# Optimization experiments

Hardware: AMD Instinct MI355X
Metric: run time of the kernel (lower is better)

## Reference

```python
import jax, jax.numpy as jnp
import numpy as np

B, N, M = 4, 1024, 1024
PFD, AD, GFD = 1024, 256, 512
H, DH = 4, 64
NR, CUT = 16, 2.0
SCALE = DH ** -0.5
OFFSETS = jnp.linspace(0.0, CUT, NR)
COEFF = -0.5 / (CUT / (NR - 1)) ** 2


def _ln(x, g, b, eps=1e-5):
    mu = x.mean(-1, keepdims=True)
    var = ((x - mu) ** 2).mean(-1, keepdims=True)
    return (x - mu) / jnp.sqrt(var + eps) * g + b


def _kabsch(src, tgt, w):
    # weighted Kabsch: rotation/translation aligning src -> tgt
    w = w / (w.sum(-1, keepdims=True) + 1e-8)  # (B,N)
    cs = jnp.einsum('bn,bnc->bc', w, src)
    ct = jnp.einsum('bn,bnc->bc', w, tgt)
    sc = src - cs[:, None]
    tc = tgt - ct[:, None]
    Hm = jnp.einsum('bn,bnc,bnd->bcd', w, sc, tc)  # (B,3,3)
    U, _, Vt = jnp.linalg.svd(Hm)
    V = jnp.swapaxes(Vt, -1, -2)
    d = jnp.linalg.det(V @ jnp.swapaxes(U, -1, -2))
    D = jnp.stack([jnp.ones_like(d), jnp.ones_like(d), d], -1)  # (B,3)
    R = jnp.einsum('bij,bj,bkj->bik', V, D, U)
    t = ct - jnp.einsum('bij,bj->bi', R, cs)
    return R, t


def setup_inputs():
    key = jax.random.key(0)
    it = iter(jax.random.split(key, 48))
    nrm = lambda s, sc=1.0: jax.random.normal(next(it), s, jnp.float32) * sc
    return {
        'src_point_feats': nrm((B, N, PFD)),
        'tgt_point_feats': nrm((B, M, PFD)),
        'src_points': nrm((B, N, 3)),
        'tgt_points': nrm((B, M, 3)),
        'tgt_global': nrm((B, GFD)),
        'sfp_w': nrm((PFD, AD), 0.02), 'sfp_b': jnp.zeros((AD,)), 'sfp_g': jnp.ones((AD,)), 'sfp_bb': jnp.zeros((AD,)),
        'tfp_w': nrm((PFD, AD), 0.02), 'tfp_b': jnp.zeros((AD,)), 'tfp_g': jnp.ones((AD,)), 'tfp_bb': jnp.zeros((AD,)),
        'rbf_w': nrm((NR, H), 0.1),
        'qw': nrm((AD, AD), 0.02), 'qb': jnp.zeros((AD,)),
        'kw': nrm((AD, AD), 0.02), 'kb': jnp.zeros((AD,)),
        'vw': nrm((AD, AD), 0.02), 'vb': jnp.zeros((AD,)),
        'ow': nrm((AD, AD), 0.02), 'ob': jnp.zeros((AD,)),
        'n1_g': jnp.ones((AD,)), 'n1_b': jnp.zeros((AD,)),
        'f1_w': nrm((AD, 4 * AD), 0.02), 'f1_b': jnp.zeros((4 * AD,)),
        'f2_w': nrm((4 * AD, AD), 0.02), 'f2_b': jnp.zeros((AD,)),
        'n2_g': jnp.ones((AD,)), 'n2_b': jnp.zeros((AD,)),
        'scp_w': nrm((AD, AD), 0.02), 'scp_b': jnp.zeros((AD,)),
        'tcp_w': nrm((AD, AD), 0.02), 'tcp_b': jnp.zeros((AD,)),
        'temperature': jnp.array(0.05, jnp.float32),
        'gp_w': nrm((AD, GFD), 0.02), 'gp_b': jnp.zeros((GFD,)), 'gp_g': jnp.ones((GFD,)), 'gp_bb': jnp.zeros((GFD,)),
    }


def reference(src_point_feats, tgt_point_feats, src_points, tgt_points, tgt_global,
              sfp_w, sfp_b, sfp_g, sfp_bb, tfp_w, tfp_b, tfp_g, tfp_bb, rbf_w,
              qw, qb, kw, kb, vw, vb, ow, ob, n1_g, n1_b,
              f1_w, f1_b, f2_w, f2_b, n2_g, n2_b,
              scp_w, scp_b, tcp_w, tcp_b, temperature,
              gp_w, gp_b, gp_g, gp_bb):
    # feature projections
    src_proj = jax.nn.relu(_ln(src_point_feats @ sfp_w + sfp_b, sfp_g, sfp_bb))  # (B,N,AD)
    tgt_proj = jax.nn.relu(_ln(tgt_point_feats @ tfp_w + tfp_b, tfp_g, tfp_bb))  # (B,M,AD)
    # inter-cloud geometric bias: cdist -> gaussian RBF -> per-head linear (dist no-grad)
    d2 = ((src_points ** 2).sum(-1)[:, :, None] + (tgt_points ** 2).sum(-1)[:, None, :]
          - 2.0 * jnp.einsum('bnc,bmc->bnm', src_points, tgt_points))
    dist = jnp.sqrt(jnp.clip(d2, 0.0))  # (B,N,M)
    rbf = jnp.exp(COEFF * (dist[..., None] - OFFSETS) ** 2)  # (B,N,M,NR)
    rbf = jax.lax.stop_gradient(rbf)
    bias = jnp.einsum('bnmr,rh->bhnm', rbf, rbf_w)
    # cross attention with geo bias (pre-LN on both streams, shared LN params)
    xq = _ln(src_proj, n1_g, n1_b)
    xc = _ln(tgt_proj, n1_g, n1_b)
    q = (xq @ qw + qb).reshape(B, N, H, DH)
    k = (xc @ kw + kb).reshape(B, M, H, DH)
    v = (xc @ vw + vb).reshape(B, M, H, DH)
    logits = jnp.einsum('bnhd,bmhd->bhnm', q, k) * SCALE + bias
    p = jax.nn.softmax(logits, axis=-1)
    attn_out = jnp.einsum('bhnm,bmhd->bnhd', p, v).reshape(B, N, AD) @ ow + ob
    x = src_proj + attn_out
    # FFN block (exact GELU as in torch)
    h = _ln(x, n2_g, n2_b)
    x = x + (jax.nn.gelu(h @ f1_w + f1_b, approximate=False) @ f2_w + f2_b)
    # soft correspondences + 3-step log-domain Sinkhorn
    src_corr = x @ scp_w + scp_b
    tgt_corr = tgt_proj @ tcp_w + tcp_b
    tau = jnp.clip(temperature, 0.01, 1.0)
    logS = jnp.einsum('bnd,bmd->bnm', src_corr, tgt_corr) / tau
    for _ in range(3):
        logS = logS - jax.nn.logsumexp(logS, axis=-1, keepdims=True)
        logS = logS - jax.nn.logsumexp(logS, axis=-2, keepdims=True)
    S = jnp.exp(logS)
    tgt_corr_points = jnp.einsum('bnm,bmc->bnc', S, tgt_points)
    confidence = S.max(-1)
    R_res, t_res = _kabsch(src_points, tgt_corr_points, confidence)
    src_global_new = jax.nn.relu(_ln(x.max(1) @ gp_w + gp_b, gp_g, gp_bb))
    combined = jnp.concatenate([src_global_new, tgt_global], axis=-1)
    return R_res, t_res, combined, confidence, S
```

## Files before the change

### kernel.cpp

```cpp
#include <hip/hip_runtime.h>
#include <hip/hip_bf16.h>
#include <math.h>

constexpr int Bn  = 4;
constexpr int Nn  = 1024;
constexpr int Mmm = 1024;
constexpr int PFDc = 1024;
constexpr int ADc  = 256;
constexpr int GFDc = 512;
constexpr int Hc   = 4;
constexpr int NRc  = 16;
constexpr int NSPLIT = 32;
constexpr float COEFFc = -28.125f;
constexpr float SCALEc = 0.125f;
constexpr float STEPc  = 2.0f / 15.0f;

__device__ __forceinline__ float addf(float a, float b) { return a + b; }
__device__ __forceinline__ double addd(double a, double b) { return a + b; }

#define BLK_REDUCE_F(OP, VAR, RES) \
  red[tid] = (VAR); __syncthreads(); \
  for (int st_ = 128; st_ > 0; st_ >>= 1) { if (tid < st_) red[tid] = OP(red[tid], red[tid + st_]); __syncthreads(); } \
  (RES) = red[0]; __syncthreads();

// ... 54 lines not shown
      float v = acc[i][j] + bias[c];
      if (addsrc) v += addsrc[(size_t)r * Cc + c];
      if (act == 1) v = 0.5f * v * (1.f + erff(v * 0.70710678118654752f));
      C[(size_t)r * Cc + c] = v;
    }
  }
}

__global__ __launch_bounds__(256) void gemm256_k(
    const float* __restrict__ A, const float* __restrict__ W, const float* __restrict__ bias,
    const float* __restrict__ addsrc, float* __restrict__ C,
    int R, int K, int Cc, int act)
{
  __shared__ __align__(16) float As[2][16][68];
  __shared__ __align__(16) float Ws[2][16][68];
  const int tid = threadIdx.x;
  const int tx = tid & 15, ty = tid >> 4;
  const int r0 = blockIdx.y * 64, c0 = blockIdx.x * 64;
  float acc[4][4] = {};
  float ra[4], rb[4];

  #pragma unroll
  for (int j = 0; j < 4; ++j) {
    int e = tid + j * 256;
    ra[j] = A[(size_t)(r0 + (e >> 4)) * K + (e & 15)];
    rb[j] = W[(size_t)(e >> 6) * Cc + c0 + (e & 63)];
  }
  #pragma unroll
  for (int j = 0; j < 4; ++j) {
    int e = tid + j * 256;
    As[0][e & 15][e >> 4] = ra[j];
    Ws[0][e >> 6][e & 63] = rb[j];
  }
  __syncthreads();

  const int nstep = K >> 4;
  for (int s = 0; s < nstep; ++s) {
    const int cur = s & 1;
    if (s + 1 < nstep) {
      const int k0 = (s + 1) << 4;
      #pragma unroll
      for (int j = 0; j < 4; ++j) {
        int e = tid + j * 256;
        ra[j] = A[(size_t)(r0 + (e >> 4)) * K + k0 + (e & 15)];
        rb[j] = W[(size_t)(k0 + (e >> 6)) * Cc + c0 + (e & 63)];
      }
    }
    #pragma unroll
    for (int kk = 0; kk < 16; ++kk) {
      float4 av = *(const float4*)&As[cur][kk][ty * 4];
      float4 wv = *(const float4*)&Ws[cur][kk][tx * 4];
      float a[4] = {av.x, av.y, av.z, av.w};
      float w[4] = {wv.x, wv.y, wv.z, wv.w};
      #pragma unroll
      for (int i = 0; i < 4; ++i)
        #pragma unroll
        for (int j = 0; j < 4; ++j)
          acc[i][j] = fmaf(a[i], w[j], acc[i][j]);
    }
    if (s + 1 < nstep) {
      #pragma unroll
      for (int j = 0; j < 4; ++j) {
        int e = tid + j * 256;
        As[cur ^ 1][e & 15][e >> 4] = ra[j];
        Ws[cur ^ 1][e >> 6][e & 63] = rb[j];
      }
    }
    __syncthreads();
  }
  #pragma unroll
  for (int i = 0; i < 4; ++i) {
    int r = r0 + ty * 4 + i;
    #pragma unroll
    for (int j = 0; j < 4; ++j) {
      int c = c0 + tx * 4 + j;
      float v = acc[i][j] + bias[c];
      if (addsrc) v += addsrc[(size_t)r * Cc + c];
      if (act == 1) v = 0.5f * v * (1.f + erff(v * 0.70710678118654752f));
      C[(size_t)r * Cc + c] = v;
    }
  }
}

__global__ __launch_bounds__(256) void gemm128_k(
    const float* __restrict__ A, const float* __restrict__ W, const float* __restrict__ bias,
    const float* __restrict__ addsrc, float* __restrict__ C,
    int R, int K, int Cc, int act)
{
  __shared__ __align__(16) float As[2][8][132];
  __shared__ __align__(16) float Ws[2][8][132];
  const int tid = threadIdx.x;
  const int tx = tid & 15, ty = tid >> 4;
  const int r0 = blockIdx.y * 128, c0 = blockIdx.x * 128;
  float acc[8][8] = {};
  float ra[4], rb[4];

  #pragma unroll
  for (int j = 0; j < 4; ++j) {
    int e = tid + j * 256;
    ra[j] = A[(size_t)(r0 + (e >> 3)) * K + (e & 7)];
    rb[j] = W[(size_t)(e >> 7) * Cc + c0 + (e & 127)];
  }
  #pragma unroll
  for (int j = 0; j < 4; ++j) {
    int e = tid + j * 256;
    As[0][e & 7][e >> 3] = ra[j];
    Ws[0][e >> 7][e & 127] = rb[j];
  }
  __syncthreads();

  const int nstep = K >> 3;
  for (int s = 0; s < nstep; ++s) {
    const int cur = s & 1;
    if (s + 1 < nstep) {
      const int k0 = (s + 1) << 3;
      #pragma unroll
      for (int j = 0; j < 4; ++j) {
        int e = tid + j * 256;
        ra[j] = A[(size_t)(r0 + (e >> 3)) * K + k0 + (e & 7)];
        rb[j] = W[(size_t)(k0 + (e >> 7)) * Cc + c0 + (e & 127)];
      }
    }
    #pragma unroll
    for (int kk = 0; kk < 8; ++kk) {
      float a[8], w[8];
      *(float4*)&a[0] = *(const float4*)&As[cur][kk][ty * 8];
      *(float4*)&a[4] = *(const float4*)&As[cur][kk][ty * 8 + 4];
      *(float4*)&w[0] = *(const float4*)&Ws[cur][kk][tx * 8];
      *(float4*)&w[4] = *(const float4*)&Ws[cur][kk][tx * 8 + 4];
      #pragma unroll
      for (int i = 0; i < 8; ++i)
        #pragma unroll
        for (int j = 0; j < 8; ++j)
          acc[i][j] = fmaf(a[i], w[j], acc[i][j]);
    }
    if (s + 1 < nstep) {
      #pragma unroll
      for (int j = 0; j < 4; ++j) {
        int e = tid + j * 256;
        As[cur ^ 1][e & 7][e >> 3] = ra[j];
        Ws[cur ^ 1][e >> 7][e & 127] = rb[j];
      }
    }
    __syncthreads();
  }
  #pragma unroll
  for (int i = 0; i < 8; ++i) {
    int r = r0 + ty * 8 + i;
    #pragma unroll
    for (int j = 0; j < 8; ++j) {
      int c = c0 + tx * 8 + j;
      float v = acc[i][j] + bias[c];
      if (addsrc) v += addsrc[(size_t)r * Cc + c];
      if (act == 1) v = 0.5f * v * (1.f + erff(v * 0.70710678118654752f));
      C[(size_t)r * Cc + c] = v;
    }
  }
}

__global__ __launch_bounds__(256) void gemm_nt128_k(
    const float* __restrict__ A, const float* __restrict__ Bm, float* __restrict__ C,
    const float* __restrict__ temp)
{
  const int K = ADc;
  __shared__ __align__(16) float As[2][8][132];
  __shared__ __align__(16) float Bs[2][8][132];
  const int tid = threadIdx.x;
  const int tx = tid & 15, ty = tid >> 4;
  const int b = blockIdx.z;
  const int r0 = blockIdx.y * 128, c0 = blockIdx.x * 128;
  const float* Ab = A + (size_t)b * Nn * K;
  const float* Bb = Bm + (size_t)b * Mmm * K;
  float* Cb = C + (size_t)b * Nn * Mmm;
  float tau = fminf(fmaxf(temp[0], 0.01f), 1.0f);
  float inv_tau = 1.f / tau;
  float acc[8][8] = {};
  float ra[4], rb[4];

  #pragma unroll
  for (int j = 0; j < 4; ++j) {
    int e = tid + j * 256;
    ra[j] = Ab[(size_t)(r0 + (e >> 3)) * K + (e & 7)];
    rb[j] = Bb[(size_t)(c0 + (e >> 3)) * K + (e & 7)];
  }
  #pragma unroll
  for (int j = 0; j < 4; ++j) {
    int e = tid + j * 256;
    As[0][e & 7][e >> 3] = ra[j];
    Bs[0][e & 7][e >> 3] = rb[j];
  }
  __syncthreads();

  const int nstep = K >> 3;
  for (int s = 0; s < nstep; ++s) {
    const int cur = s & 1;
    if (s + 1 < nstep) {
      const int k0 = (s + 1) << 3;
      #pragma unroll
      for (int j = 0; j < 4; ++j) {
        int e = tid + j * 256;
        ra[j] = Ab[(size_t)(r0 + (e >> 3)) * K + k0 + (e & 7)];
        rb[j] = Bb[(size_t)(c0 + (e >> 3)) * K + k0 + (e & 7)];
      }
    }
    #pragma unroll
    for (int kk = 0; kk < 8; ++kk) {
      float a[8], w[8];
      *(float4*)&a[0] = *(const float4*)&As[cur][kk][ty * 8];
      *(float4*)&a[4] = *(const float4*)&As[cur][kk][ty * 8 + 4];
      *(float4*)&w[0] = *(const float4*)&Bs[cur][kk][tx * 8];
      *(float4*)&w[4] = *(const float4*)&Bs[cur][kk][tx * 8 + 4];
      #pragma unroll
      for (int i = 0; i < 8; ++i)
        #pragma unroll
        for (int j = 0; j < 8; ++j)
          acc[i][j] = fmaf(a[i], w[j], acc[i][j]);
    }
    if (s + 1 < nstep) {
      #pragma unroll
      for (int j = 0; j < 4; ++j) {
        int e = tid + j * 256;
        As[cur ^ 1][e & 7][e >> 3] = ra[j];
        Bs[cur ^ 1][e & 7][e >> 3] = rb[j];
      }
    }
    __syncthreads();
  }
  #pragma unroll
  for (int i = 0; i < 8; ++i) {
    int r = r0 + ty * 8 + i;
    #pragma unroll
    for (int j = 0; j < 8; ++j) {
      int c = c0 + tx * 8 + j;
      Cb[(size_t)r * Mmm + c] = acc[i][j] * inv_tau;
    }
  }
}

__global__ __launch_bounds__(256) void ln_k(
    const float* __restrict__ in, const float* __restrict__ g, const float* __restrict__ bb,
    float* __restrict__ out, int Cc, int relu)
{
  const int tid = threadIdx.x;
  const int row = blockIdx.x;
  const float* x = in + (size_t)row * Cc;
  float* o = out + (size_t)row * Cc;
  __shared__ float red[256];
  float s = 0.f;
  for (int j = tid; j < Cc; j += 256) s += x[j];
  float tot; BLK_REDUCE_F(addf, s, tot);
  float mu = tot / Cc;
  float s2 = 0.f;
  for (int j = tid; j < Cc; j += 256) { float d = x[j] - mu; s2 += d * d; }
  float tot2; BLK_REDUCE_F(addf, s2, tot2);
  float inv = 1.f / sqrtf(tot2 / Cc + 1e-5f);
  for (int j = tid; j < Cc; j += 256) {
    float v = (x[j] - mu) * inv * g[j] + bb[j];
    if (relu) v = fmaxf(v, 0.f);
    o[j] = v;
  }
}

__global__ __launch_bounds__(256) void ln2_k(
    const float* __restrict__ in, const float* __restrict__ g, const float* __restrict__ bb,
    float* __restrict__ out, int relu)
{
  const int row = blockIdx.x;
  const int tid = threadIdx.x;
  float x = in[(size_t)row * 256 + tid];
  float s = x, s2 = x * x;
  #pragma unroll
  for (int off = 32; off > 0; off >>= 1) {
    s  += __shfl_xor(s, off, 64);
    s2 += __shfl_xor(s2, off, 64);
  }
  __shared__ float as_[4], as2_[4];
  const int wv = tid >> 6, ln = tid & 63;
  if (ln == 0) { as_[wv] = s; as2_[wv] = s2; }
  __syncthreads();
  s  = as_[0] + as_[1] + as_[2] + as_[3];
  s2 = as2_[0] + as2_[1] + as2_[2] + as2_[3];
  float mu = s * (1.f / 256.f);
  float var = fmaxf(s2 * (1.f / 256.f) - mu * mu, 0.f);
  float inv = 1.f / sqrtf(var + 1e-5f);
  float v = (x - mu) * inv * g[tid] + bb[tid];
  if (relu) v = fmaxf(v, 0.f);
  out[(size_t)row * 256 + tid] = v;
}

__global__ __launch_bounds__(256) void fattn(
    const float* __restrict__ q, const float* __restrict__ k, const float* __restrict__ v,
    const float* __restrict__ src_pts, const float* __restrict__ tgt_pts,
    const float* __restrict__ rbfw, float* __restrict__ ctx)
{
  const int bh = blockIdx.x;
  const int b = bh >> 2, h = bh & 3;
  const int n0 = blockIdx.y * 32;
  const int tid = threadIdx.x;
  const int tx = tid & 15, ty = tid >> 4;
  const int lane = tid & 63, w = tid >> 6;
  const int mml = lane >> 4;
  const int dd  = lane & 15;

  __shared__ __align__(16) float Qs[64][36];
  __shared__ __align__(16) float Ks[64][68];
  __shared__ __align__(16) float Vs[64][68];
  __shared__ __align__(16) float Ps[32][68];
  __shared__ float spx[32], spy[32], spz[32];
  __shared__ float tpx[64], tpy[64], tpz[64];
  __shared__ float rw[16];

  #pragma unroll
  for (int c = 0; c < 8; ++c) {
    int n = c * 4 + mml;
    int d = w * 16 + dd;
    Qs[d][n] = q[((size_t)b * Nn + n0 + n) * ADc + h * 64 + d];
  }
  if (tid < 32) {
    spx[tid] = src_pts[((size_t)b * Nn + n0 + tid) * 3 + 0];
    spy[tid] = src_pts[((size_t)b * Nn + n0 + tid) * 3 + 1];
    spz[tid] = src_pts[((size_t)b * Nn + n0 + tid) * 3 + 2];
  }
  if (tid < 16) rw[tid] = rbfw[tid * Hc + h];

  float O[2][4] = {};
  float mrun[2] = {-1e30f, -1e30f};
  float lrun[2] = {0.f, 0.f};

  for (int t = 0; t < Mmm / 64; ++t) {
    const int m0 = t * 64;
    __syncthreads();
    #pragma unroll
    for (int c = 0; c < 16; ++c) {
      int mm = c * 4 + mml;
      int d = w * 16 + dd;
      Ks[d][mm] = k[((size_t)b * Mmm + m0 + mm) * ADc + h * 64 + d];
    }
    #pragma unroll
    for (int c = 0; c < 16; ++c) {
      int mm = c * 4 + w;
      Vs[mm][lane] = v[((size_t)b * Mmm + m0 + mm) * ADc + h * 64 + lane];
    }
    if (tid < 64) {
      tpx[tid] = tgt_pts[((size_t)b * Mmm + m0 + tid) * 3 + 0];
      tpy[tid] = tgt_pts[((size_t)b * Mmm + m0 + tid) * 3 + 1];
      tpz[tid] = tgt_pts[((size_t)b * Mmm + m0 + tid) * 3 + 2];
    }
    __syncthreads();

    float S[2][4] = {};
    #pragma unroll
    for (int d = 0; d < 64; ++d) {
      float2 qv = *(const float2*)&Qs[d][ty * 2];
      float4 kv = *(const float4*)&Ks[d][tx * 4];
      float kw[4] = {kv.x, kv.y, kv.z, kv.w};
      #pragma unroll
      for (int j = 0; j < 4; ++j) {
        S[0][j] = fmaf(qv.x, kw[j], S[0][j]);
        S[1][j] = fmaf(qv.y, kw[j], S[1][j]);
      }
    }

    #pragma unroll
    for (int i = 0; i < 2; ++i) {
      int n = ty * 2 + i;
      float s0 = spx[n], s1 = spy[n], s2 = spz[n];
      float sq = s0 * s0 + s1 * s1 + s2 * s2;
      float rmx = -1e30f;
      #pragma unroll
      for (int j = 0; j < 4; ++j) {
        int mj = tx * 4 + j;
        float t0 = tpx[mj], t1 = tpy[mj], t2 = tpz[mj];
        float d2 = sq + t0 * t0 + t1 * t1 + t2 * t2 - 2.f * (s0 * t0 + s1 * t1 + s2 * t2);
        float dist = sqrtf(fmaxf(d2, 0.f));
        float bias = 0.f;
        float dq = dist;
        #pragma unroll
        for (int r = 0; r < NRc; ++r) {
          bias = fmaf(__expf(COEFFc * dq * dq), rw[r], bias);
          dq -= STEPc;
        }
        float lv = S[i][j] * SCALEc + bias;
        S[i][j] = lv;
        rmx = fmaxf(rmx, lv);
      }
      #pragma unroll
      for (int off = 1; off < 16; off <<= 1)
        rmx = fmaxf(rmx, __shfl_xor(rmx, off, 64));
      float mn = fmaxf(mrun[i], rmx);
      float alpha = __expf(mrun[i] - mn);
      mrun[i] = mn;
      float p0 = __expf(S[i][0] - mn);
      float p1 = __expf(S[i][1] - mn);
      float p2 = __expf(S[i][2] - mn);
      float p3 = __expf(S[i][3] - mn);
      *(float4*)&Ps[n][tx * 4] = make_float4(p0, p1, p2, p3);
      float rs = p0 + p1 + p2 + p3;
      #pragma unroll
      for (int off = 1; off < 16; off <<= 1)
        rs += __shfl_xor(rs, off, 64);
      lrun[i] = lrun[i] * alpha + rs;
      O[i][0] *= alpha; O[i][1] *= alpha; O[i][2] *= alpha; O[i][3] *= alpha;
    }

    #pragma unroll
    for (int m = 0; m < 64; ++m) {
      float4 vv = *(const float4*)&Vs[m][tx * 4];
      float vw[4] = {vv.x, vv.y, vv.z, vv.w};
      float p0 = Ps[ty * 2][m];
      float p1 = Ps[ty * 2 + 1][m];
      #pragma unroll
      for (int j = 0; j < 4; ++j) {
        O[0][j] = fmaf(p0, vw[j], O[0][j]);
        O[1][j] = fmaf(p1, vw[j], O[1][j]);
      }
    }
  }

  #pragma unroll
  for (int i = 0; i < 2; ++i) {
    int n = n0 + ty * 2 + i;
    float invl = 1.f / lrun[i];
    size_t base = ((size_t)b * Nn + n) * ADc + h * 64 + tx * 4;
    ctx[base + 0] = O[i][0] * invl;
    ctx[base + 1] = O[i][1] * invl;
    ctx[base + 2] = O[i][2] * invl;
    ctx[base + 3] = O[i][3] * invl;
  }
}

__global__ __launch_bounds__(256) void row_lse2_k(float* __restrict__ logS, const float* __restrict__ colLse)
{
  const int tid = threadIdx.x;
  const int bn = blockIdx.x;
  const int b = bn >> 10;
  float* row = logS + (size_t)bn * Mmm;
  float4 v4 = *(float4*)&row[tid * 4];
  if (colLse) {
    const float4 c4 = *(const float4*)&colLse[(size_t)b * Mmm + tid * 4];
    v4.x -= c4.x; v4.y -= c4.y; v4.z -= c4.z; v4.w -= c4.w;
  }
  float mx = fmaxf(fmaxf(v4.x, v4.y), fmaxf(v4.z, v4.w));
  float sm = __expf(v4.x - mx) + __expf(v4.y - mx) + __expf(v4.z - mx) + __expf(v4.w - mx);
  #pragma unroll
  for (int off = 32; off > 0; off >>= 1) {
    float mo = __shfl_xor(mx, off, 64);
    float so = __shfl_xor(sm, off, 64);
    float mn = fmaxf(mx, mo);
    sm = sm * __expf(mx - mn) + so * __expf(mo - mn);
    mx = mn;
  }
  __shared__ float wm[4], wsum[4];
  const int wv = tid >> 6, ln = tid & 63;
  if (ln == 0) { wm[wv] = mx; wsum[wv] = sm; }
  __syncthreads();
  float m0 = fmaxf(fmaxf(wm[0], wm[1]), fmaxf(wm[2], wm[3]));
  float stot = wsum[0] * __expf(wm[0] - m0) + wsum[1] * __expf(wm[1] - m0)
             + wsum[2] * __expf(wm[2] - m0) + wsum[3] * __expf(wm[3] - m0);
  float lse = m0 + __logf(stot);
  v4.x -= lse; v4.y -= lse; v4.z -= lse; v4.w -= lse;
  *(float4*)&row[tid * 4] = v4;
}

__global__ __launch_bounds__(256) void col_part_k(
    const float* __restrict__ logS, float* __restrict__ pmax, float* __restrict__ psum)
{
  const int b = blockIdx.z, sp = blockIdx.y;
  const int m = blockIdx.x * 256 + threadIdx.x;
  const int RPS = Nn / NSPLIT;
  const float* base = logS + ((size_t)b * Nn + sp * RPS) * Mmm + m;
  float mx = -1e30f, sm = 0.f;
  for (int i = 0; i < RPS; ++i) {
    float v = base[(size_t)i * Mmm];
    if (v > mx) { sm = sm * __expf(mx - v) + 1.f; mx = v; }
    else sm += __expf(v - mx);
  }
  size_t o = ((size_t)b * NSPLIT + sp) * Mmm + m;
  pmax[o] = mx; psum[o] = sm;
}

__global__ __launch_bounds__(256) void col_comb_k(
    const float* __restrict__ pmax, const float* __restrict__ psum, float* __restrict__ colLse)
{
  const int b = blockIdx.y;
  const int m = blockIdx.x * 256 + threadIdx.x;
  float mx = -1e30f;
  for (int s = 0; s < NSPLIT; ++s) mx = fmaxf(mx, pmax[((size_t)b * NSPLIT + s) * Mmm + m]);
  float sm = 0.f;
  for (int s = 0; s < NSPLIT; ++s) {
    size_t o = ((size_t)b * NSPLIT + s) * Mmm + m;
    sm += psum[o] * __expf(pmax[o] - mx);
  }
  colLse[(size_t)b * Mmm + m] = mx + __logf(sm);
}

__global__ __launch_bounds__(256) void finalize_k(
    const float* __restrict__ logS, const float* __restrict__ colLse,
// ... 208 lines not shown
  const int b = blockIdx.x, ch = blockIdx.y;
  const int d = threadIdx.x;
  float mx = -1e30f;
  const int n0 = ch * 64;
  for (int n = n0; n < n0 + 64; ++n)
    mx = fmaxf(mx, x[((size_t)b * Nn + n) * ADc + d]);
  part[((size_t)b * 16 + ch) * ADc + d] = mx;
}

__global__ __launch_bounds__(256) void xmax_comb_k(const float* __restrict__ part, float* __restrict__ xmax)
{
  const int b = blockIdx.x, d = threadIdx.x;
  float mx = -1e30f;
  for (int c = 0; c < 16; ++c) mx = fmaxf(mx, part[((size_t)b * 16 + c) * ADc + d]);
  xmax[(size_t)b * ADc + d] = mx;
}

__global__ __launch_bounds__(256) void combined_k(
    const float* __restrict__ gl, const float* __restrict__ tgt_global, float* __restrict__ outC)
{
  int i = blockIdx.x * 256 + threadIdx.x;
  int b = i >> 10, j = i & 1023;
  float v = (j < GFDc) ? gl[(size_t)b * GFDc + j] : tgt_global[(size_t)b * GFDc + (j - GFDc)];
  outC[i] = v;
}

extern "C" void kernel_launch(void* const* d_in, const int* in_sizes, int n_in,
                              void* d_out, int out_size, void* d_ws, size_t ws_size,
                              hipStream_t stream) {
  (void)in_sizes; (void)n_in; (void)out_size; (void)ws_size;
  const float* src_feats = (const float*)d_in[0];
  const float* tgt_feats = (const float*)d_in[1];
  const float* src_pts   = (const float*)d_in[2];
  const float* tgt_pts   = (const float*)d_in[3];
  const float* tgt_glob  = (const float*)d_in[4];
  const float* sfp_w = (const float*)d_in[5];  const float* sfp_b = (const float*)d_in[6];
  const float* sfp_g = (const float*)d_in[7];  const float* sfp_bb = (const float*)d_in[8];
  const float* tfp_w = (const float*)d_in[9];  const float* tfp_b = (const float*)d_in[10];
  const float* tfp_g = (const float*)d_in[11]; const float* tfp_bb = (const float*)d_in[12];
  const float* rbf_w = (const float*)d_in[13];
  const float* qw = (const float*)d_in[14]; const float* qb = (const float*)d_in[15];
  const float* kw = (const float*)d_in[16]; const float* kb = (const float*)d_in[17];
  const float* vw = (const float*)d_in[18]; const float* vb = (const float*)d_in[19];
  const float* ow = (const float*)d_in[20]; const float* ob = (const float*)d_in[21];
  const float* n1_g = (const float*)d_in[22]; const float* n1_b = (const float*)d_in[23];
  const float* f1_w = (const float*)d_in[24]; const float* f1_b = (const float*)d_in[25];
  const float* f2_w = (const float*)d_in[26]; const float* f2_b = (const float*)d_in[27];
  const float* n2_g = (const float*)d_in[28]; const float* n2_b = (const float*)d_in[29];
  const float* scp_w = (const float*)d_in[30]; const float* scp_b = (const float*)d_in[31];
  const float* tcp_w = (const float*)d_in[32]; const float* tcp_b = (const float*)d_in[33];
  const float* temp  = (const float*)d_in[34];
  const float* gp_w = (const float*)d_in[35]; const float* gp_b = (const float*)d_in[36];
  const float* gp_g = (const float*)d_in[37]; const float* gp_bb = (const float*)d_in[38];

  float* out = (float*)d_out;
  float* outR    = out;
  float* outT    = out + 36;
  float* outC    = out + 48;
  float* outConf = out + 48 + 4096;
  float* outS    = out + 48 + 4096 + 4096;

  float* ws = (float*)d_ws;
  const size_t M1 = 1048576;
  float* A_   = ws + 0 * M1;
  float* B_   = ws + 1 * M1;
  float* C_   = ws + 2 * M1;
  float* D_   = ws + 3 * M1;
  float* E_   = ws + 4 * M1;
  float* F_   = ws + 5 * M1;
  float* G_   = ws + 6 * M1;
  float* logS = ws + 0 * M1;
  float* hid  = ws + 1 * M1;
  float* tail = ws + 7 * M1;
  float* colLse = tail;
  float* pmax   = colLse + 4096;
  float* psum   = pmax + 131072;
  float* conf   = psum + 131072;
  float* tcp    = conf + 4096;
  float* xmax   = tcp + 12288;
  float* glraw  = xmax + 1024;
  float* gl     = glraw + 2048;
  double* kab   = (double*)(gl + 2048);
  float* xpart  = (float*)(kab + 64);

  const int BN = Bn * Nn;

  gemm256_k<<<dim3(ADc / 64, BN / 64), 256, 0, stream>>>(src_feats, sfp_w, sfp_b, nullptr, A_, BN, PFDc, ADc, 0);
  ln2_k<<<BN, 256, 0, stream>>>(A_, sfp_g, sfp_bb, G_, 1);
  gemm256_k<<<dim3(ADc / 64, BN / 64), 256, 0, stream>>>(tgt_feats, tfp_w, tfp_b, nullptr, A_, BN, PFDc, ADc, 0);
  ln2_k<<<BN, 256, 0, stream>>>(A_, tfp_g, tfp_bb, F_, 1);

  ln2_k<<<BN, 256, 0, stream>>>(G_, n1_g, n1_b, A_, 0);
  gemm256_k<<<dim3(ADc / 64, BN / 64), 256, 0, stream>>>(A_, qw, qb, nullptr, C_, BN, ADc, ADc, 0);
  ln2_k<<<BN, 256, 0, stream>>>(F_, n1_g, n1_b, B_, 0);
  gemm256_k<<<dim3(ADc / 64, BN / 64), 256, 0, stream>>>(B_, kw, kb, nullptr, E_, BN, ADc, ADc, 0);
  gemm256_k<<<dim3(ADc / 64, BN / 64), 256, 0, stream>>>(B_, vw, vb, nullptr, D_, BN, ADc, ADc, 0);

  fattn<<<dim3(Bn * Hc, Nn / 32), 256, 0, stream>>>(C_, E_, D_, src_pts, tgt_pts, rbf_w, B_);
  gemm256_k<<<dim3(ADc / 64, BN / 64), 256, 0, stream>>>(B_, ow, ob, G_, G_, BN, ADc, ADc, 0);

  ln2_k<<<BN, 256, 0, stream>>>(G_, n2_g, n2_b, A_, 0);
  gemm128_k<<<dim3(1024 / 128, BN / 128), 256, 0, stream>>>(A_, f1_w, f1_b, nullptr, hid, BN, ADc, 1024, 1);
  gemm256_k<<<dim3(ADc / 64, BN / 64), 256, 0, stream>>>(hid, f2_w, f2_b, G_, G_, BN, 1024, ADc, 0);

  gemm256_k<<<dim3(ADc / 64, BN / 64), 256, 0, stream>>>(G_, scp_w, scp_b, nullptr, E_, BN, ADc, ADc, 0);

  xmax_part_k<<<dim3(Bn, 16), 256, 0, stream>>>(G_, xpart);
  xmax_comb_k<<<Bn, 256, 0, stream>>>(xpart, xmax);
  gemm_k<<<dim3(GFDc / 64, 1), 256, 0, stream>>>(xmax, gp_w, gp_b, nullptr, glraw, Bn, ADc, GFDc, 0);
  ln_k<<<Bn, 256, 0, stream>>>(glraw, gp_g, gp_bb, gl, GFDc, 1);
  combined_k<<<(Bn * 2 * GFDc) / 256, 256, 0, stream>>>(gl, tgt_glob, outC);

  gemm256_k<<<dim3(ADc / 64, BN / 64), 256, 0, stream>>>(F_, tcp_w, tcp_b, nullptr, G_, BN, ADc, ADc, 0);
  gemm_nt128_k<<<dim3(Mmm / 128, Nn / 128, Bn), 256, 0, stream>>>(E_, G_, logS, temp);

  for (int it = 0; it < 3; ++it) {
    row_lse2_k<<<BN, 256, 0, stream>>>(logS, it == 0 ? nullptr : colLse);
    col_part_k<<<dim3(Mmm / 256, NSPLIT, Bn), 256, 0, stream>>>(logS, pmax, psum);
    col_comb_k<<<dim3(Mmm / 256, Bn), 256, 0, stream>>>(pmax, psum, colLse);
  }
  finalize_k<<<BN, 256, 0, stream>>>(logS, colLse, tgt_pts, outS, outConf, conf, tcp);

  kabsch_red_k<<<Bn, 256, 0, stream>>>(conf, src_pts, tcp, kab);
  kabsch_svd_k<<<1, 64, 0, stream>>>(kab, outR, outT);
}
```

Before: 828.8 us.

## Split-K projection GEMMs, fuse K/V GEMM, tabulate RBF bias, prefetch attention tiles

The K=1024 GEMMs (input projections and FFN down-projection) become split-K into four partial buffers, which a fused reduce+bias+LayerNorm or reduce+residual kernel then combines. This raises block count for the narrow 256-column outputs. K and V weights are packed once so one GEMM produces both, and the FFN up-projection and Sinkhorn logits GEMM move to 64x64 tiles. The attention kernel replaces the 16-term RBF exp sum with a per-block lookup table and linear interpolation, and register-prefetches the next K/V tile. The cost is extra partial-buffer traffic and a small approximation error in the RBF bias.

```diff
diff --git a/kernel.cpp b/kernel.cpp
--- a/kernel.cpp
+++ b/kernel.cpp
@@ -160,156 +160,198 @@
   }
 }
 
-__global__ __launch_bounds__(256) void gemm128_k(
-    const float* __restrict__ A, const float* __restrict__ W, const float* __restrict__ bias,
-    const float* __restrict__ addsrc, float* __restrict__ C,
-    int R, int K, int Cc, int act)
-{
-  __shared__ __align__(16) float As[2][8][132];
-  __shared__ __align__(16) float Ws[2][8][132];
+__global__ __launch_bounds__(256) void gemm_sk_k(
+    const float* __restrict__ A, const float* __restrict__ W, float* __restrict__ P)
+{
+  __shared__ __align__(16) float As[2][16][68];
+  __shared__ __align__(16) float Ws[2][16][68];
   const int tid = threadIdx.x;
   const int tx = tid & 15, ty = tid >> 4;
-  const int r0 = blockIdx.y * 128, c0 = blockIdx.x * 128;
-  float acc[8][8] = {};
+  const int r0 = blockIdx.y * 64, c0 = blockIdx.x * 64;
+  const int koff = blockIdx.z * 256;
+  float acc[4][4] = {};
   float ra[4], rb[4];
 
   #pragma unroll
   for (int j = 0; j < 4; ++j) {
     int e = tid + j * 256;
-    ra[j] = A[(size_t)(r0 + (e >> 3)) * K + (e & 7)];
-    rb[j] = W[(size_t)(e >> 7) * Cc + c0 + (e & 127)];
+    ra[j] = A[(size_t)(r0 + (e >> 4)) * 1024 + koff + (e & 15)];
+    rb[j] = W[(size_t)(koff + (e >> 6)) * 256 + c0 + (e & 63)];
   }
   #pragma unroll
   for (int j = 0; j < 4; ++j) {
     int e = tid + j * 256;
-    As[0][e & 7][e >> 3] = ra[j];
-    Ws[0][e >> 7][e & 127] = rb[j];
+    As[0][e & 15][e >> 4] = ra[j];
+    Ws[0][e >> 6][e & 63] = rb[j];
   }
   __syncthreads();
 
-  const int nstep = K >> 3;
-  for (int s = 0; s < nstep; ++s) {
+  for (int s = 0; s < 16; ++s) {
     const int cur = s & 1;
-    if (s + 1 < nstep) {
-      const int k0 = (s + 1) << 3;
+    if (s + 1 < 16) {
+      const int k0 = koff + ((s + 1) << 4);
       #pragma unroll
       for (int j = 0; j < 4; ++j) {
         int e = tid + j * 256;
-        ra[j] = A[(size_t)(r0 + (e >> 3)) * K + k0 + (e & 7)];
-        rb[j] = W[(size_t)(k0 + (e >> 7)) * Cc + c0 + (e & 127)];
-      }
-    }
-    #pragma unroll
-    for (int kk = 0; kk < 8; ++kk) {
-      float a[8], w[8];
-      *(float4*)&a[0] = *(const float4*)&As[cur][kk][ty * 8];
-      *(float4*)&a[4] = *(const float4*)&As[cur][kk][ty * 8 + 4];
-      *(float4*)&w[0] = *(const float4*)&Ws[cur][kk][tx * 8];
-      *(float4*)&w[4] = *(const float4*)&Ws[cur][kk][tx * 8 + 4];
-      #pragma unroll
-      for (int i = 0; i < 8; ++i)
+        ra[j] = A[(size_t)(r0 + (e >> 4)) * 1024 + k0 + (e & 15)];
+        rb[j] = W[(size_t)(k0 + (e >> 6)) * 256 + c0 + (e & 63)];
+      }
+    }
+    #pragma unroll
+    for (int kk = 0; kk < 16; ++kk) {
+      float4 av = *(const float4*)&As[cur][kk][ty * 4];
+      float4 wv = *(const float4*)&Ws[cur][kk][tx * 4];
+      float a[4] = {av.x, av.y, av.z, av.w};
+      float w[4] = {wv.x, wv.y, wv.z, wv.w};
+      #pragma unroll
+      for (int i = 0; i < 4; ++i)
         #pragma unroll
-        for (int j = 0; j < 8; ++j)
+        for (int j = 0; j < 4; ++j)
           acc[i][j] = fmaf(a[i], w[j], acc[i][j]);
     }
-    if (s + 1 < nstep) {
+    if (s + 1 < 16) {
       #pragma unroll
       for (int j = 0; j < 4; ++j) {
         int e = tid + j * 256;
-        As[cur ^ 1][e & 7][e >> 3] = ra[j];
-        Ws[cur ^ 1][e >> 7][e & 127] = rb[j];
+        As[cur ^ 1][e & 15][e >> 4] = ra[j];
+        Ws[cur ^ 1][e >> 6][e & 63] = rb[j];
       }
     }
     __syncthreads();
   }
-  #pragma unroll
-  for (int i = 0; i < 8; ++i) {
-    int r = r0 + ty * 8 + i;
-    #pragma unroll
-    for (int j = 0; j < 8; ++j) {
-      int c = c0 + tx * 8 + j;
-      float v = acc[i][j] + bias[c];
-      if (addsrc) v += addsrc[(size_t)r * Cc + c];
-      if (act == 1) v = 0.5f * v * (1.f + erff(v * 0.70710678118654752f));
-      C[(size_t)r * Cc + c] = v;
-    }
-  }
-}
-
-__global__ __launch_bounds__(256) void gemm_nt128_k(
+  float* Pz = P + (size_t)blockIdx.z * 1048576;
+  #pragma unroll
+  for (int i = 0; i < 4; ++i) {
+    int r = r0 + ty * 4 + i;
+    #pragma unroll
+    for (int j = 0; j < 4; ++j)
+      Pz[(size_t)r * 256 + c0 + tx * 4 + j] = acc[i][j];
+  }
+}
+
+__global__ __launch_bounds__(256) void ln4_k(
+    const float* __restrict__ p, const float* __restrict__ bias,
+    const float* __restrict__ g, const float* __restrict__ bb,
+    float* __restrict__ out, int relu)
+{
+  const int row = blockIdx.x;
+  const int tid = threadIdx.x;
+  size_t o = (size_t)row * 256 + tid;
+  float x = p[o] + p[o + 1048576] + p[o + 2097152] + p[o + 3145728] + bias[tid];
+  float s = x, s2 = x * x;
+  #pragma unroll
+  for (int off = 32; off > 0; off >>= 1) {
+    s  += __shfl_xor(s, off, 64);
+    s2 += __shfl_xor(s2, off, 64);
+  }
+  __shared__ float as_[4], as2_[4];
+  const int wv = tid >> 6, ln = tid & 63;
+  if (ln == 0) { as_[wv] = s; as2_[wv] = s2; }
+  __syncthreads();
+  s  = as_[0] + as_[1] + as_[2] + as_[3];
+  s2 = as2_[0] + as2_[1] + as2_[2] + as2_[3];
+  float mu = s * (1.f / 256.f);
+  float var = fmaxf(s2 * (1.f / 256.f) - mu * mu, 0.f);
+  float inv = 1.f / sqrtf(var + 1e-5f);
+  float v = (x - mu) * inv * g[tid] + bb[tid];
+  if (relu) v = fmaxf(v, 0.f);
+  out[o] = v;
+}
+
+__global__ __launch_bounds__(256) void red4_k(
+    const float* __restrict__ p, const float* __restrict__ bias, float* __restrict__ out)
+{
+  size_t i = (size_t)blockIdx.x * 256 + threadIdx.x;
+  out[i] += p[i] + p[i + 1048576] + p[i + 2097152] + p[i + 3145728] + bias[threadIdx.x];
+}
+
+__global__ __launch_bounds__(256) void pack_kv_k(
+    const float* __restrict__ kw, const float* __restrict__ kb,
+    const float* __restrict__ vw, const float* __restrict__ vb,
+    float* __restrict__ kvw, float* __restrict__ kvb)
+{
+  int i = blockIdx.x * 256 + threadIdx.x;
+  if (i < 256 * 512) {
+    int r = i >> 9, c = i & 511;
+    kvw[i] = (c < 256) ? kw[r * 256 + c] : vw[r * 256 + (c - 256)];
+  } else if (i < 256 * 512 + 512) {
+    int c = i - 256 * 512;
+    kvb[c] = (c < 256) ? kb[c] : vb[c - 256];
+  }
+}
+
+__global__ __launch_bounds__(256) void gemm_nt256_k(
     const float* __restrict__ A, const float* __restrict__ Bm, float* __restrict__ C,
     const float* __restrict__ temp)
 {
   const int K = ADc;
-  __shared__ __align__(16) float As[2][8][132];
-  __shared__ __align__(16) float Bs[2][8][132];
+  __shared__ __align__(16) float As[2][16][68];
+  __shared__ __align__(16) float Bs[2][16][68];
   const int tid = threadIdx.x;
   const int tx = tid & 15, ty = tid >> 4;
   const int b = blockIdx.z;
-  const int r0 = blockIdx.y * 128, c0 = blockIdx.x * 128;
+  const int r0 = blockIdx.y * 64, c0 = blockIdx.x * 64;
   const float* Ab = A + (size_t)b * Nn * K;
   const float* Bb = Bm + (size_t)b * Mmm * K;
   float* Cb = C + (size_t)b * Nn * Mmm;
   float tau = fminf(fmaxf(temp[0], 0.01f), 1.0f);
   float inv_tau = 1.f / tau;
-  float acc[8][8] = {};
+  float acc[4][4] = {};
   float ra[4], rb[4];
 
   #pragma unroll
   for (int j = 0; j < 4; ++j) {
     int e = tid + j * 256;
-    ra[j] = Ab[(size_t)(r0 + (e >> 3)) * K + (e & 7)];
-    rb[j] = Bb[(size_t)(c0 + (e >> 3)) * K + (e & 7)];
+    ra[j] = Ab[(size_t)(r0 + (e >> 4)) * K + (e & 15)];
+    rb[j] = Bb[(size_t)(c0 + (e >> 4)) * K + (e & 15)];
   }
   #pragma unroll
   for (int j = 0; j < 4; ++j) {
     int e = tid + j * 256;
-    As[0][e & 7][e >> 3] = ra[j];
-    Bs[0][e & 7][e >> 3] = rb[j];
+    As[0][e & 15][e >> 4] = ra[j];
+    Bs[0][e & 15][e >> 4] = rb[j];
   }
   __syncthreads();
 
-  const int nstep = K >> 3;
-  for (int s = 0; s < nstep; ++s) {
+  for (int s = 0; s < 16; ++s) {
     const int cur = s & 1;
-    if (s + 1 < nstep) {
-      const int k0 = (s + 1) << 3;
+    if (s + 1 < 16) {
+      const int k0 = (s + 1) << 4;
       #pragma unroll
       for (int j = 0; j < 4; ++j) {
         int e = tid + j * 256;
-        ra[j] = Ab[(size_t)(r0 + (e >> 3)) * K + k0 + (e & 7)];
-        rb[j] = Bb[(size_t)(c0 + (e >> 3)) * K + k0 + (e & 7)];
-      }
-    }
-    #pragma unroll
-    for (int kk = 0; kk < 8; ++kk) {
-      float a[8], w[8];
-      *(float4*)&a[0] = *(const float4*)&As[cur][kk][ty * 8];
-      *(float4*)&a[4] = *(const float4*)&As[cur][kk][ty * 8 + 4];
-      *(float4*)&w[0] = *(const float4*)&Bs[cur][kk][tx * 8];
-      *(float4*)&w[4] = *(const float4*)&Bs[cur][kk][tx * 8 + 4];
-      #pragma unroll
-      for (int i = 0; i < 8; ++i)
+        ra[j] = Ab[(size_t)(r0 + (e >> 4)) * K + k0 + (e & 15)];
+        rb[j] = Bb[(size_t)(c0 + (e >> 4)) * K + k0 + (e & 15)];
+      }
+    }
+    #pragma unroll
+    for (int kk = 0; kk < 16; ++kk) {
+      float4 av = *(const float4*)&As[cur][kk][ty * 4];
+      float4 wv = *(const float4*)&Bs[cur][kk][tx * 4];
+      float a[4] = {av.x, av.y, av.z, av.w};
+      float w[4] = {wv.x, wv.y, wv.z, wv.w};
+      #pragma unroll
+      for (int i = 0; i < 4; ++i)
         #pragma unroll
-        for (int j = 0; j < 8; ++j)
+        for (int j = 0; j < 4; ++j)
           acc[i][j] = fmaf(a[i], w[j], acc[i][j]);
     }
-    if (s + 1 < nstep) {
+    if (s + 1 < 16) {
       #pragma unroll
       for (int j = 0; j < 4; ++j) {
         int e = tid + j * 256;
-        As[cur ^ 1][e & 7][e >> 3] = ra[j];
-        Bs[cur ^ 1][e & 7][e >> 3] = rb[j];
+        As[cur ^ 1][e & 15][e >> 4] = ra[j];
+        Bs[cur ^ 1][e & 15][e >> 4] = rb[j];
       }
     }
     __syncthreads();
   }
   #pragma unroll
-  for (int i = 0; i < 8; ++i) {
-    int r = r0 + ty * 8 + i;
-    #pragma unroll
-    for (int j = 0; j < 8; ++j) {
-      int c = c0 + tx * 8 + j;
+  for (int i = 0; i < 4; ++i) {
+    int r = r0 + ty * 4 + i;
+    #pragma unroll
+    for (int j = 0; j < 4; ++j) {
+      int c = c0 + tx * 4 + j;
       Cb[(size_t)r * Mmm + c] = acc[i][j] * inv_tau;
     }
   }
@@ -367,7 +409,7 @@
 }
 
 __global__ __launch_bounds__(256) void fattn(
-    const float* __restrict__ q, const float* __restrict__ k, const float* __restrict__ v,
+    const float* __restrict__ q, const float* __restrict__ kv,
     const float* __restrict__ src_pts, const float* __restrict__ tgt_pts,
     const float* __restrict__ rbfw, float* __restrict__ ctx)
 {
@@ -387,7 +429,9 @@
   __shared__ float spx[32], spy[32], spz[32];
   __shared__ float tpx[64], tpy[64], tpz[64];
   __shared__ float rw[16];
-
+  __shared__ float Tb[2048];
+
+  if (tid < 16) rw[tid] = rbfw[tid * Hc + h];
   #pragma unroll
   for (int c = 0; c < 8; ++c) {
     int n = c * 4 + mml;
@@ -399,30 +443,59 @@
     spy[tid] = src_pts[((size_t)b * Nn + n0 + tid) * 3 + 1];
     spz[tid] = src_pts[((size_t)b * Nn + n0 + tid) * 3 + 2];
   }
-  if (tid < 16) rw[tid] = rbfw[tid * Hc + h];
+  __syncthreads();
+
+  for (int i = tid; i < 2048; i += 256) {
+    float di = (float)i * (1.0f / 512.0f);
+    float s = 0.f;
+    #pragma unroll
+    for (int r = 0; r < NRc; ++r) {
+      float dq = di - STEPc * r;
+      s = fmaf(__expf(COEFFc * dq * dq), rw[r], s);
+    }
+    Tb[i] = s;
+  }
+
+  float kreg[16], vreg[16];
+  float tp0 = 0.f, tp1 = 0.f, tp2 = 0.f;
+  {
+    const size_t kb_ = ((size_t)b * Mmm) * 512 + h * 64;
+    #pragma unroll
+    for (int c = 0; c < 16; ++c) {
+      kreg[c] = kv[kb_ + (size_t)(c * 4 + mml) * 512 + w * 16 + dd];
+      vreg[c] = kv[kb_ + (size_t)(c * 4 + w) * 512 + 256 + lane];
+    }
+    if (tid < 64) {
+      tp0 = tgt_pts[((size_t)b * Mmm + tid) * 3 + 0];
+      tp1 = tgt_pts[((size_t)b * Mmm + tid) * 3 + 1];
+      tp2 = tgt_pts[((size_t)b * Mmm + tid) * 3 + 2];
+    }
+  }
 
   float O[2][4] = {};
   float mrun[2] = {-1e30f, -1e30f};
   float lrun[2] = {0.f, 0.f};
 
   for (int t = 0; t < Mmm / 64; ++t) {
-    const int m0 = t * 64;
     __syncthreads();
     #pragma unroll
-    for (int c = 0; c < 16; ++c) {
-      int mm = c * 4 + mml;
-      int d = w * 16 + dd;
-      Ks[d][mm] = k[((size_t)b * Mmm + m0 + mm) * ADc + h * 64 + d];
-    }
-    #pragma unroll
-    for (int c = 0; c < 16; ++c) {
-      int mm = c * 4 + w;
-      Vs[mm][lane] = v[((size_t)b * Mmm + m0 + mm) * ADc + h * 64 + lane];
-    }
-    if (tid < 64) {
-      tpx[tid] = tgt_pts[((size_t)b * Mmm + m0 + tid) * 3 + 0];
-      tpy[tid] = tgt_pts[((size_t)b * Mmm + m0 + tid) * 3 + 1];
-      tpz[tid] = tgt_pts[((size_t)b * Mmm + m0 + tid) * 3 + 2];
+    for (int c = 0; c < 16; ++c) Ks[w * 16 + dd][c * 4 + mml] = kreg[c];
+    #pragma unroll
+    for (int c = 0; c < 16; ++c) Vs[c * 4 + w][lane] = vreg[c];
+    if (tid < 64) { tpx[tid] = tp0; tpy[tid] = tp1; tpz[tid] = tp2; }
+    if (t + 1 < Mmm / 64) {
+      const size_t kb_ = ((size_t)b * Mmm + (t + 1) * 64) * 512 + h * 64;
+      #pragma unroll
+      for (int c = 0; c < 16; ++c) {
+        kreg[c] = kv[kb_ + (size_t)(c * 4 + mml) * 512 + w * 16 + dd];
+        vreg[c] = kv[kb_ + (size_t)(c * 4 + w) * 512 + 256 + lane];
+      }
+      if (tid < 64) {
+        size_t tb_ = ((size_t)b * Mmm + (t + 1) * 64 + tid) * 3;
+        tp0 = tgt_pts[tb_ + 0];
+        tp1 = tgt_pts[tb_ + 1];
+        tp2 = tgt_pts[tb_ + 2];
+      }
     }
     __syncthreads();
 
@@ -430,12 +503,12 @@
     #pragma unroll
     for (int d = 0; d < 64; ++d) {
       float2 qv = *(const float2*)&Qs[d][ty * 2];
-      float4 kv = *(const float4*)&Ks[d][tx * 4];
-      float kw[4] = {kv.x, kv.y, kv.z, kv.w};
+      float4 kv4 = *(const float4*)&Ks[d][tx * 4];
+      float kwv[4] = {kv4.x, kv4.y, kv4.z, kv4.w};
       #pragma unroll
       for (int j = 0; j < 4; ++j) {
-        S[0][j] = fmaf(qv.x, kw[j], S[0][j]);
-        S[1][j] = fmaf(qv.y, kw[j], S[1][j]);
+        S[0][j] = fmaf(qv.x, kwv[j], S[0][j]);
+        S[1][j] = fmaf(qv.y, kwv[j], S[1][j]);
       }
     }
 
@@ -451,13 +524,12 @@
         float t0 = tpx[mj], t1 = tpy[mj], t2 = tpz[mj];
         float d2 = sq + t0 * t0 + t1 * t1 + t2 * t2 - 2.f * (s0 * t0 + s1 * t1 + s2 * t2);
         float dist = sqrtf(fmaxf(d2, 0.f));
-        float bias = 0.f;
-        float dq = dist;
-        #pragma unroll
-        for (int r = 0; r < NRc; ++r) {
-          bias = fmaf(__expf(COEFFc * dq * dq), rw[r], bias);
-          dq -= STEPc;
-        }
+        float fidx = fminf(dist * 512.0f, 2047.0f);
+        int i0 = (int)fidx;
+        i0 = (i0 > 2046) ? 2046 : i0;
+        float frac = fidx - (float)i0;
+        float b0 = Tb[i0];
+        float bias = fmaf(Tb[i0 + 1] - b0, frac, b0);
         float lv = S[i][j] * SCALEc + bias;
         S[i][j] = lv;
         rmx = fmaxf(rmx, lv);
@@ -484,13 +556,13 @@
     #pragma unroll
     for (int m = 0; m < 64; ++m) {
       float4 vv = *(const float4*)&Vs[m][tx * 4];
-      float vw[4] = {vv.x, vv.y, vv.z, vv.w};
+      float vwv[4] = {vv.x, vv.y, vv.z, vv.w};
       float p0 = Ps[ty * 2][m];
       float p1 = Ps[ty * 2 + 1][m];
       #pragma unroll
       for (int j = 0; j < 4; ++j) {
-        O[0][j] = fmaf(p0, vw[j], O[0][j]);
-        O[1][j] = fmaf(p1, vw[j], O[1][j]);
+        O[0][j] = fmaf(p0, vwv[j], O[0][j]);
+        O[1][j] = fmaf(p1, vwv[j], O[1][j]);
       }
     }
   }
@@ -865,28 +937,32 @@
   float* gl     = glraw + 2048;
   double* kab   = (double*)(gl + 2048);
   float* xpart  = (float*)(kab + 64);
+  float* kvw    = pmax;
+  float* kvb    = psum;
 
   const int BN = Bn * Nn;
 
-  gemm256_k<<<dim3(ADc / 64, BN / 64), 256, 0, stream>>>(src_feats, sfp_w, sfp_b, nullptr, A_, BN, PFDc, ADc, 0);
-  ln2_k<<<BN, 256, 0, stream>>>(A_, sfp_g, sfp_bb, G_, 1);
-  gemm256_k<<<dim3(ADc / 64, BN / 64), 256, 0, stream>>>(tgt_feats, tfp_w, tfp_b, nullptr, A_, BN, PFDc, ADc, 0);
-  ln2_k<<<BN, 256, 0, stream>>>(A_, tfp_g, tfp_bb, F_, 1);
+  pack_kv_k<<<514, 256, 0, stream>>>(kw, kb, vw, vb, kvw, kvb);
+
+  gemm_sk_k<<<dim3(4, 64, 4), 256, 0, stream>>>(src_feats, sfp_w, outS);
+  ln4_k<<<BN, 256, 0, stream>>>(outS, sfp_b, sfp_g, sfp_bb, G_, 1);
+  gemm_sk_k<<<dim3(4, 64, 4), 256, 0, stream>>>(tgt_feats, tfp_w, outS);
+  ln4_k<<<BN, 256, 0, stream>>>(outS, tfp_b, tfp_g, tfp_bb, F_, 1);
 
   ln2_k<<<BN, 256, 0, stream>>>(G_, n1_g, n1_b, A_, 0);
-  gemm256_k<<<dim3(ADc / 64, BN / 64), 256, 0, stream>>>(A_, qw, qb, nullptr, C_, BN, ADc, ADc, 0);
+  gemm256_k<<<dim3(4, 64), 256, 0, stream>>>(A_, qw, qb, nullptr, C_, BN, ADc, ADc, 0);
   ln2_k<<<BN, 256, 0, stream>>>(F_, n1_g, n1_b, B_, 0);
-  gemm256_k<<<dim3(ADc / 64, BN / 64), 256, 0, stream>>>(B_, kw, kb, nullptr, E_, BN, ADc, ADc, 0);
-  gemm256_k<<<dim3(ADc / 64, BN / 64), 256, 0, stream>>>(B_, vw, vb, nullptr, D_, BN, ADc, ADc, 0);
-
-  fattn<<<dim3(Bn * Hc, Nn / 32), 256, 0, stream>>>(C_, E_, D_, src_pts, tgt_pts, rbf_w, B_);
-  gemm256_k<<<dim3(ADc / 64, BN / 64), 256, 0, stream>>>(B_, ow, ob, G_, G_, BN, ADc, ADc, 0);
+  gemm256_k<<<dim3(8, 64), 256, 0, stream>>>(B_, kvw, kvb, nullptr, D_, BN, ADc, 512, 0);
+
+  fattn<<<dim3(Bn * Hc, Nn / 32), 256, 0, stream>>>(C_, D_, src_pts, tgt_pts, rbf_w, B_);
+  gemm256_k<<<dim3(4, 64), 256, 0, stream>>>(B_, ow, ob, G_, G_, BN, ADc, ADc, 0);
 
   ln2_k<<<BN, 256, 0, stream>>>(G_, n2_g, n2_b, A_, 0);
-  gemm128_k<<<dim3(1024 / 128, BN / 128), 256, 0, stream>>>(A_, f1_w, f1_b, nullptr, hid, BN, ADc, 1024, 1);
-  gemm256_k<<<dim3(ADc / 64, BN / 64), 256, 0, stream>>>(hid, f2_w, f2_b, G_, G_, BN, 1024, ADc, 0);
-
-  gemm256_k<<<dim3(ADc / 64, BN / 64), 256, 0, stream>>>(G_, scp_w, scp_b, nullptr, E_, BN, ADc, ADc, 0);
+  gemm256_k<<<dim3(16, 64), 256, 0, stream>>>(A_, f1_w, f1_b, nullptr, hid, BN, ADc, 1024, 1);
+  gemm_sk_k<<<dim3(4, 64, 4), 256, 0, stream>>>(hid, f2_w, outS);
+  red4_k<<<BN, 256, 0, stream>>>(outS, f2_b, G_);
+
+  gemm256_k<<<dim3(4, 64), 256, 0, stream>>>(G_, scp_w, scp_b, nullptr, E_, BN, ADc, ADc, 0);
 
   xmax_part_k<<<dim3(Bn, 16), 256, 0, stream>>>(G_, xpart);
   xmax_comb_k<<<Bn, 256, 0, stream>>>(xpart, xmax);
@@ -894,8 +970,8 @@
   ln_k<<<Bn, 256, 0, stream>>>(glraw, gp_g, gp_bb, gl, GFDc, 1);
   combined_k<<<(Bn * 2 * GFDc) / 256, 256, 0, stream>>>(gl, tgt_glob, outC);
 
-  gemm256_k<<<dim3(ADc / 64, BN / 64), 256, 0, stream>>>(F_, tcp_w, tcp_b, nullptr, G_, BN, ADc, ADc, 0);
-  gemm_nt128_k<<<dim3(Mmm / 128, Nn / 128, Bn), 256, 0, stream>>>(E_, G_, logS, temp);
+  gemm256_k<<<dim3(4, 64), 256, 0, stream>>>(F_, tcp_w, tcp_b, nullptr, G_, BN, ADc, ADc, 0);
+  gemm_nt256_k<<<dim3(16, 16, Bn), 256, 0, stream>>>(E_, G_, logS, temp);
 
   for (int it = 0; it < 3; ++it) {
     row_lse2_k<<<BN, 256, 0, stream>>>(logS, it == 0 ? nullptr : colLse);
```

Measured after the change: 743.2 us. 10.3% less time.
